# Performance work log

Hardware: AMD Instinct MI355X
Metric: run time of the kernel (lower is better)

The kernel has to match this reference:

```python
import jax, jax.numpy as jnp
import numpy as np

B, L, C, H = 32, 641, 768, 12
MEM = 128  # memory slots K; state token at index K; tokens are causal after that


def _block_mask(L, K):
    # rows i attend to cols j per FusedAttention:
    #  memory rows (i<K): attend to memory+state (j<=K)
    #  state row (i==K): attends to everything
    #  token rows (i>K): attend to memory+state (j<=K) and causally to tokens (K<j<=i)
    i = jnp.arange(L)[:, None]
    j = jnp.arange(L)[None, :]
    mem_rows = (i < K) & (j <= K)
    state_row = (i == K)
    tok_rows = (i > K) & ((j <= K) | ((j > K) & (j <= i)))
    return mem_rows | state_row | tok_rows  # (L, L) bool


def setup_inputs() -> dict:
    key = jax.random.key(0)
    k1, k2, k3 = jax.random.split(key, 3)
    x = jax.random.normal(k1, (B, L, C), dtype=jnp.float32)
    W_attn = jax.random.normal(k2, (C, 3 * C), dtype=jnp.float32) * 0.02
    W_proj = jax.random.normal(k3, (C, C), dtype=jnp.float32) * 0.02
    return {"x": x, "W_attn": W_attn, "W_proj": W_proj, "mem_size": MEM}


def reference(x, W_attn, W_proj, mem_size):
    Bb, Ll, Cc = x.shape
    hd = Cc // H
    qkv = x @ W_attn  # (B, L, 3C)
    q, k, v = jnp.split(qkv, 3, axis=-1)
    # (B, H, L, hd)
    q = q.reshape(Bb, Ll, H, hd).transpose(0, 2, 1, 3)
    k = k.reshape(Bb, Ll, H, hd).transpose(0, 2, 1, 3)
    v = v.reshape(Bb, Ll, H, hd).transpose(0, 2, 1, 3)
    mask = _block_mask(Ll, mem_size)  # (L, L)
    scale = 1.0 / jnp.sqrt(jnp.asarray(hd, dtype=x.dtype))
    att = jnp.einsum("bhqd,bhkd->bhqk", q, k) * scale
    att = jnp.where(mask[None, None, :, :], att, jnp.asarray(-jnp.inf, att.dtype))
    att = jax.nn.softmax(att, axis=-1)
    y = jnp.einsum("bhqk,bhkd->bhqd", att, v)
    y = y.transpose(0, 2, 1, 3).reshape(Bb, Ll, Cc)
    return y @ W_proj
```

## Files before the change

kernel.cpp:

```cpp
#include <hip/hip_runtime.h>
#include <stdint.h>

#define B_SZ 32
#define L_SZ 641
#define C_SZ 768
#define H_SZ 12
#define HD 64
#define MEMK 128
#define M_REAL (B_SZ * L_SZ)
#define M_PAD 20608
#define N_QKV (3 * C_SZ)
#define NQP 6
#define QK_STRIDE 1536
#define VT_STRIDE 648
#define SCL_LOG2E 0.18033688f
#define FIXED_MAX 8.0f

typedef __attribute__((ext_vector_type(8))) short short8;
typedef __attribute__((ext_vector_type(4))) float f32x4;
typedef __attribute__((ext_vector_type(4))) unsigned short ushort4v;

__device__ inline unsigned short f2bf(float x) {
  union { float f; uint32_t u; } v; v.f = x;
  uint32_t r = v.u + 0x7fffu + ((v.u >> 16) & 1u);
  return (unsigned short)(r >> 16);
}
__device__ inline float bf2f(short v) {
  union { float f; uint32_t u; } x; x.u = ((uint32_t)(unsigned short)v) << 16;
  return x.f;
}

__device__ inline void gload_lds16(const void* g, void* l) {
  __builtin_amdgcn_global_load_lds(
      (const __attribute__((address_space(1))) uint32_t*)g,
      (__attribute__((address_space(3))) uint32_t*)l, 16, 0, 0);
}

__global__ __launch_bounds__(256) void k_conv_x(const float* __restrict__ src,
                                                unsigned short* __restrict__ dst,
                                                int n4) {
  int i = blockIdx.x * 256 + threadIdx.x;
  if (i >= n4) return;
  float4 v = *(const float4*)(src + (size_t)i * 4);
  ushort4v o = { f2bf(v.x), f2bf(v.y), f2bf(v.z), f2bf(v.w) };
  int m = (unsigned)i / 192u;
  int k = (i - m * 192) * 4;
  int kk = k ^ ((m & 7) << 3);
  *(ushort4v*)(dst + (size_t)m * C_SZ + kk) = o;
}

__global__ __launch_bounds__(256) void k_transpose_bf16(const float* __restrict__ src,
                                                        unsigned short* __restrict__ dst,
                                                        int R, int Ccol,
                                                        float scale, int scale_cmax) {
  __shared__ float tile[32][33];
  int c0 = blockIdx.x * 32, r0 = blockIdx.y * 32;
  int tx = threadIdx.x & 31, ty = threadIdx.x >> 5;
  for (int i = ty; i < 32; i += 8)
    tile[i][tx] = src[(size_t)(r0 + i) * Ccol + c0 + tx];
  __syncthreads();
  float sc = (c0 < scale_cmax) ? scale : 1.0f;
  for (int i = ty; i < 32; i += 8) {
    int c = c0 + i;
    int r = (r0 + tx) ^ ((c & 7) << 3);
    dst[(size_t)c * R + r] = f2bf(tile[tx][i] * sc);
  }
}

template <int MODE>
__global__ __launch_bounds__(256) void k_gemm(const short* __restrict__ A,
                                              const short* __restrict__ Bt,
                                              void* __restrict__ Cp,
                                              short* __restrict__ vt,
                                              int Mreal, int N, int K) {
  __shared__ short As[2][128 * 64];
  __shared__ short Bs[2][128 * 64];
  int nwg = gridDim.x;
  int qq = nwg >> 3, rr = nwg & 7;
  int x8 = blockIdx.x & 7, i8 = blockIdx.x >> 3;
  int wg = (x8 < rr ? x8 * (qq + 1) : rr * (qq + 1) + (x8 - rr) * qq) + i8;
  const int tiles_n = N >> 7;
  int tm = wg / tiles_n, tn = wg % tiles_n;
  int m0 = tm << 7, n0 = tn << 7;
  int lane = threadIdx.x & 63, wave = threadIdx.x >> 6;
  int wr = wave >> 1, wc = wave & 1;
  int l15 = lane & 15, g = lane >> 4;
  int gswz = (l15 & 7) << 4;

  f32x4 acc[4][4];
  f32x4 z = {0.f, 0.f, 0.f, 0.f};
#pragma unroll
  for (int i = 0; i < 4; ++i)
#pragma unroll
    for (int j = 0; j < 4; ++j) acc[i][j] = z;

  int arow = lane >> 3;
  int acol = (lane & 7) * 8;

#define STAGE(K0, BUF)                                                        \
  {                                                                           \
    _Pragma("unroll")                                                         \
    for (int cc = 0; cc < 4; ++cc) {                                          \
      int rb = (cc * 4 + wave) * 8;                                           \
      gload_lds16(A + (size_t)(m0 + rb + arow) * K + ((K0) + acol),           \
                  (char*)As[BUF] + rb * 128);                                 \
      gload_lds16(Bt + (size_t)(n0 + rb + arow) * K + ((K0) + acol),          \
                  (char*)Bs[BUF] + rb * 128);                                 \
    }                                                                         \
  }

  STAGE(0, 0);
  STAGE(64, 1);
  int nk = K >> 6;
  for (int t = 0; t < nk; ++t) {
    int buf = t & 1;
    if (t + 1 < nk) {
      asm volatile("s_waitcnt vmcnt(8)" ::: "memory");
    } else {
      asm volatile("s_waitcnt vmcnt(0)" ::: "memory");
    }
    __builtin_amdgcn_s_barrier();
#pragma unroll
    for (int ks = 0; ks < 2; ++ks) {
      short8 a[4], b[4];
      int roff = (ks * 64) ^ gswz;
      if (MODE == 3) {
#pragma unroll
        for (int nf = 0; nf < 4; ++nf)
          a[nf] = *(const short8*)((char*)Bs[buf] +
                      (wr * 64 + nf * 16 + l15) * 128 + (roff ^ (g * 16)));
#pragma unroll
        for (int mf = 0; mf < 4; ++mf)
          b[mf] = *(const short8*)((char*)As[buf] +
                      (wc * 64 + mf * 16 + l15) * 128 + (roff ^ (g * 16)));
      } else {
#pragma unroll
        for (int mf = 0; mf < 4; ++mf)
          a[mf] = *(const short8*)((char*)As[buf] +
                      (wr * 64 + mf * 16 + l15) * 128 + (roff ^ (g * 16)));
#pragma unroll
        for (int nf = 0; nf < 4; ++nf)
          b[nf] = *(const short8*)((char*)Bs[buf] +
                      (wc * 64 + nf * 16 + l15) * 128 + (roff ^ (g * 16)));
      }
#pragma unroll
      for (int i = 0; i < 4; ++i)
#pragma unroll
        for (int j = 0; j < 4; ++j)
          acc[i][j] = __builtin_amdgcn_mfma_f32_16x16x32_bf16(a[i], b[j], acc[i][j], 0, 0, 0);
    }
    __builtin_amdgcn_s_barrier();
    __builtin_amdgcn_sched_barrier(0);
    if (t + 2 < nk) STAGE((t + 2) << 6, buf);
  }
#undef STAGE

  if (MODE == 3) {
#pragma unroll
    for (int nf = 0; nf < 4; ++nf) {
#pragma unroll
      for (int reg = 0; reg < 4; ++reg) {
        int n = n0 + wr * 64 + nf * 16 + g * 4 + reg;
        int h = n >> 6, d = n & 63;
        int xr = (d & 7) << 3;
#pragma unroll
        for (int mf = 0; mf < 4; ++mf) {
          int m = m0 + wc * 64 + mf * 16 + l15;
          if (m >= Mreal) continue;
          int bb = (unsigned)m / 641u;
          int key = m - bb * 641;
          int k2 = (key >= 640) ? key : (key ^ xr);
          vt[((size_t)(bb * H_SZ + h) * HD + d) * VT_STRIDE + k2] = f2bf(acc[nf][mf][reg]);
        }
      }
    }
    return;
  }
#pragma unroll
  for (int mf = 0; mf < 4; ++mf) {
#pragma unroll
    for (int reg = 0; reg < 4; ++reg) {
      int m = m0 + wr * 64 + mf * 16 + g * 4 + reg;
      if (m >= Mreal) continue;
      int xr = 0;
      if (MODE == 2) {
        int bb = (unsigned)m / 641u;
        int key = m - bb * 641;
        xr = (key & 7) << 3;
      }
#pragma unroll
      for (int nf = 0; nf < 4; ++nf) {
        int n = n0 + wc * 64 + nf * 16 + l15;
        float v = acc[mf][nf][reg];
        if (MODE == 2) {
          int nn = (n >= C_SZ) ? (n ^ xr) : n;
          ((unsigned short*)Cp)[(size_t)m * QK_STRIDE + nn] = f2bf(v);
        } else
          ((float*)Cp)[(size_t)m * N + n] = v;
      }
    }
  }
}

__global__ __launch_bounds__(512) void k_attn(const short* __restrict__ qk,
                                              const short* __restrict__ vt,
                                              short* __restrict__ y) {
  __shared__ short Ks[2][64 * 64];
  __shared__ short Vt[2][64 * 64];
  __shared__ short Ps[8][16 * 64];

  int bid = blockIdx.x;
  int work = (bid & 7) * 288 + (bid >> 3);
  int qp = work % NQP;
  int rem = work / NQP;
  int h = rem % H_SZ;
  int b = rem / H_SZ;
  int q0 = qp * 128;
  int tid = threadIdx.x;
  int lane = tid & 63, w = tid >> 6;
  int wgp = w >> 2;
  int l15 = lane & 15, g = lane >> 4;
  int q0w = q0 + wgp * 64 + (w & 3) * 16;

  size_t qbase = (size_t)(b * L_SZ + q0w + l15) * QK_STRIDE + h * HD;
  short8 qa[2];
#pragma unroll
  for (int ks = 0; ks < 2; ++ks)
    qa[ks] = *(const short8*)&qk[qbase + ks * 32 + g * 8];

  f32x4 o[4];
  float l_run[4];
  f32x4 z = {0.f, 0.f, 0.f, 0.f};
  f32x4 m8 = {-FIXED_MAX, -FIXED_MAX, -FIXED_MAX, -FIXED_MAX};
#pragma unroll
  for (int df = 0; df < 4; ++df) o[df] = z;
#pragma unroll
  for (int r = 0; r < 4; ++r) l_run[r] = 0.f;

  int jmax[4];
#pragma unroll
  for (int reg = 0; reg < 4; ++reg) {
    int i = q0w + g * 4 + reg;
    jmax[reg] = (i == MEMK) ? (L_SZ - 1) : (i < MEMK ? MEMK : i);
  }
  int jm_min = (q0w <= MEMK) ? MEMK : q0w;

  int q1 = q0 + 127; if (q1 > L_SZ - 1) q1 = L_SZ - 1;
  int col_max = (q0 <= MEMK && MEMK <= q1) ? (L_SZ - 1) : (q1 < MEMK ? MEMK : q1);
  int qw1 = q0w + 15;
  bool dead = (q0w >= L_SZ);
  int wcol = (q0w <= MEMK && MEMK <= qw1) ? (L_SZ - 1) : (qw1 < MEMK ? MEMK : qw1);
  if (dead) wcol = -1;

  size_t kbase = (size_t)b * L_SZ * QK_STRIDE + C_SZ + h * HD;
  size_t vbase = (size_t)(b * H_SZ + h) * HD * VT_STRIDE;

  int i0 = tid >> 3, j0e = (tid & 7) * 8;
  int rswz = (l15 & 7) << 4;

#define STAGE_ATTN(C0, BUF)                                                   \
  {                                                                           \
    gload_lds16(qk + kbase + (size_t)((C0) + i0) * QK_STRIDE + j0e,           \
                (char*)Ks[BUF] + w * 1024);                                   \
    gload_lds16(vt + vbase + (size_t)i0 * VT_STRIDE + (C0) + j0e,             \
                (char*)Vt[BUF] + w * 1024);                                   \
  }

  STAGE_ATTN(0, 0);
  STAGE_ATTN(64, 1);

  int nt = col_max >> 6;
  for (int t = 0; t <= nt; ++t) {
    int c0 = t << 6;
    int buf = t & 1;
    if (t + 1 <= nt) {
      asm volatile("s_waitcnt vmcnt(2)" ::: "memory");
    } else {
      asm volatile("s_waitcnt vmcnt(0)" ::: "memory");
    }
    __builtin_amdgcn_s_barrier();

    if (c0 <= wcol) {
      int vswz = (c0 >= 640) ? 0 : rswz;

      f32x4 s[4];
      __builtin_amdgcn_s_setprio(1);
#pragma unroll
      for (int kf = 0; kf < 4; ++kf) {
        f32x4 sa = m8;
#pragma unroll
        for (int ks = 0; ks < 2; ++ks) {
          short8 kb = *(const short8*)((char*)Ks[buf] +
                          (kf * 16 + l15) * 128 + ((ks * 64 + g * 16) ^ rswz));
          sa = __builtin_amdgcn_mfma_f32_16x16x32_bf16(qa[ks], kb, sa, 0, 0, 0);
        }
        s[kf] = sa;
      }
      __builtin_amdgcn_s_setprio(0);

      if (c0 + 63 > jm_min) {
#pragma unroll
        for (int kf = 0; kf < 4; ++kf) {
          int j = c0 + kf * 16 + l15;
#pragma unroll
          for (int reg = 0; reg < 4; ++reg)
            s[kf][reg] = (j <= jmax[reg]) ? s[kf][reg] : -1e30f;
        }
      }

#pragma unroll
      for (int kf = 0; kf < 4; ++kf)
#pragma unroll
        for (int reg = 0; reg < 4; ++reg)
          s[kf][reg] = exp2f(s[kf][reg]);
#pragma unroll
      for (int reg = 0; reg < 4; ++reg)
        l_run[reg] += (s[0][reg] + s[1][reg]) + (s[2][reg] + s[3][reg]);

#pragma unroll
      for (int reg = 0; reg < 4; ++reg) {
        int q = g * 4 + reg;
        char* prow = (char*)Ps[w] + q * 128;
        int qswz = (q & 7) << 4;
#pragma unroll
        for (int kf = 0; kf < 4; kf += 2) {
          uint32_t r;
          asm("v_cvt_pk_bf16_f32 %0, %1, %2"
              : "=v"(r) : "v"(s[kf][reg]), "v"(s[kf + 1][reg]));
          *(short*)(prow + ((kf * 32 + l15 * 2) ^ qswz)) = (short)(r & 0xffff);
          *(short*)(prow + (((kf + 1) * 32 + l15 * 2) ^ qswz)) = (short)(r >> 16);
        }
      }

      short8 pa[2];
#pragma unroll
      for (int ks = 0; ks < 2; ++ks)
        pa[ks] = *(const short8*)((char*)Ps[w] + l15 * 128 + ((ks * 64 + g * 16) ^ rswz));
      __builtin_amdgcn_s_setprio(1);
#pragma unroll
      for (int df = 0; df < 4; ++df) {
#pragma unroll
        for (int ks = 0; ks < 2; ++ks) {
          short8 vb = *(const short8*)((char*)Vt[buf] +
                          (df * 16 + l15) * 128 + ((ks * 64 + g * 16) ^ vswz));
          o[df] = __builtin_amdgcn_mfma_f32_16x16x32_bf16(pa[ks], vb, o[df], 0, 0, 0);
        }
      }
      __builtin_amdgcn_s_setprio(0);
    }

    __builtin_amdgcn_s_barrier();
    __builtin_amdgcn_sched_barrier(0);
    if (t + 2 <= nt) STAGE_ATTN((t + 2) << 6, buf);
  }
#undef STAGE_ATTN

#pragma unroll
  for (int reg = 0; reg < 4; ++reg) {
    float ls = l_run[reg];
    ls += __shfl_xor(ls, 1);
    ls += __shfl_xor(ls, 2);
    ls += __shfl_xor(ls, 4);
    ls += __shfl_xor(ls, 8);
    int i = q0w + g * 4 + reg;
    if (i >= L_SZ) continue;
    float inv = 1.0f / ls;
    size_t m = (size_t)(b * L_SZ + i);
    int ixr = ((int)(m & 7)) << 3;
#pragma unroll
    for (int df = 0; df < 4; ++df) {
      int col = (df * 16 + l15) ^ ixr;
      y[m * C_SZ + h * HD + col] = (short)f2bf(o[df][reg] * inv);
    }
  }
}

extern "C" void kernel_launch(void* const* d_in, const int* in_sizes, int n_in,
                              void* d_out, int out_size, void* d_ws, size_t ws_size,
                              hipStream_t stream) {
  const float* x = (const float*)d_in[0];
  const float* Wa = (const float*)d_in[1];
  const float* Wp = (const float*)d_in[2];
  float* out = (float*)d_out;

  char* ws = (char*)d_ws;
  size_t off0 = 0;
  short* x_bf = (short*)(ws + off0);
  size_t off1 = off0 + (size_t)M_PAD * C_SZ * 2;
  short* Wa_t = (short*)(ws + off1);
  size_t off2 = off1 + (size_t)N_QKV * C_SZ * 2;
  short* Wp_t = (short*)(ws + off2);
  size_t off3 = off2 + (size_t)C_SZ * C_SZ * 2;
  short* qk = (short*)(ws + off3);
  size_t off4 = off3 + (size_t)M_REAL * QK_STRIDE * 2;
  short* vt = (short*)(ws + off4);
  size_t need = off4 + (size_t)B_SZ * H_SZ * HD * VT_STRIDE * 2 + 4096;
  if (ws_size < need) return;

  int n4 = M_REAL * C_SZ / 4;
  k_conv_x<<<(n4 + 255) / 256, 256, 0, stream>>>(x, (unsigned short*)x_bf, n4);
  k_transpose_bf16<<<dim3(N_QKV / 32, C_SZ / 32), 256, 0, stream>>>(
      Wa, (unsigned short*)Wa_t, C_SZ, N_QKV, SCL_LOG2E, C_SZ);
  k_transpose_bf16<<<dim3(C_SZ / 32, C_SZ / 32), 256, 0, stream>>>(
      Wp, (unsigned short*)Wp_t, C_SZ, C_SZ, 1.0f, 0);

  k_gemm<2><<<(M_PAD / 128) * (QK_STRIDE / 128), 256, 0, stream>>>(
      x_bf, Wa_t, (void*)qk, nullptr, M_REAL, QK_STRIDE, C_SZ);
  k_gemm<3><<<(M_PAD / 128) * (C_SZ / 128), 256, 0, stream>>>(
      x_bf, Wa_t + (size_t)QK_STRIDE * C_SZ, nullptr, vt, M_REAL, C_SZ, C_SZ);
  k_attn<<<B_SZ * H_SZ * NQP, 512, 0, stream>>>(qk, vt, x_bf );
  k_gemm<0><<<(M_PAD / 128) * (C_SZ / 128), 256, 0, stream>>>(
      x_bf, Wp_t, (void*)out, nullptr, M_REAL, C_SZ, C_SZ);
}
```

Baseline: 242.2 us.

## Enlarge GEMM tiles to 256x256 with 512-thread workgroups

The shared GEMM kernel moves from 128x128 tiles with 4 waves to 256x256 tiles with 8 waves. Each wave now computes a 128x64 sub-tile, and A rows past M_PAD are clamped. The larger tiles raise arithmetic intensity and cut global and LDS traffic per FLOP. In exchange, LDS use rises to 128KB per block, each wave holds more accumulator registers, and the grid has far fewer workgroups, which risks lower occupancy and poor wave quantization across the CUs.

```diff
diff --git a/kernel.cpp b/kernel.cpp
--- a/kernel.cpp
+++ b/kernel.cpp
@@ -9,6 +9,7 @@
 #define MEMK 128
 #define M_REAL (B_SZ * L_SZ)
 #define M_PAD 20608
+#define MT256 81
 #define N_QKV (3 * C_SZ)
 #define NQP 6
 #define QK_STRIDE 1536
@@ -68,44 +69,46 @@
 }
 
 template <int MODE>
-__global__ __launch_bounds__(256) void k_gemm(const short* __restrict__ A,
-                                              const short* __restrict__ Bt,
-                                              void* __restrict__ Cp,
-                                              short* __restrict__ vt,
-                                              int Mreal, int N, int K) {
-  __shared__ short As[2][128 * 64];
-  __shared__ short Bs[2][128 * 64];
+__global__ __launch_bounds__(512, 2) void k_gemm(const short* __restrict__ A,
+                                                 const short* __restrict__ Bt,
+                                                 void* __restrict__ Cp,
+                                                 short* __restrict__ vt,
+                                                 int Mreal, int N, int K) {
+  __shared__ short As[2][256 * 64];
+  __shared__ short Bs[2][256 * 64];
   int nwg = gridDim.x;
   int qq = nwg >> 3, rr = nwg & 7;
   int x8 = blockIdx.x & 7, i8 = blockIdx.x >> 3;
   int wg = (x8 < rr ? x8 * (qq + 1) : rr * (qq + 1) + (x8 - rr) * qq) + i8;
-  const int tiles_n = N >> 7;
+  const int tiles_n = N >> 8;
   int tm = wg / tiles_n, tn = wg % tiles_n;
-  int m0 = tm << 7, n0 = tn << 7;
-  int lane = threadIdx.x & 63, wave = threadIdx.x >> 6;
-  int wr = wave >> 1, wc = wave & 1;
+  int m0 = tm << 8, n0 = tn << 8;
+  int tid = threadIdx.x;
+  int lane = tid & 63, wave = tid >> 6;
+  int wr = wave >> 2, wc = wave & 3;
   int l15 = lane & 15, g = lane >> 4;
   int gswz = (l15 & 7) << 4;
 
-  f32x4 acc[4][4];
+  f32x4 acc[8][4];
   f32x4 z = {0.f, 0.f, 0.f, 0.f};
 #pragma unroll
-  for (int i = 0; i < 4; ++i)
-#pragma unroll
-    for (int j = 0; j < 4; ++j) acc[i][j] = z;
-
-  int arow = lane >> 3;
-  int acol = (lane & 7) * 8;
+  for (int i2 = 0; i2 < 8; ++i2)
+#pragma unroll
+    for (int j2 = 0; j2 < 4; ++j2) acc[i2][j2] = z;
+
+  int srow = wave * 8 + (lane >> 3);
+  int scol = (lane & 7) * 8;
 
 #define STAGE(K0, BUF)                                                        \
   {                                                                           \
     _Pragma("unroll")                                                         \
-    for (int cc = 0; cc < 4; ++cc) {                                          \
-      int rb = (cc * 4 + wave) * 8;                                           \
-      gload_lds16(A + (size_t)(m0 + rb + arow) * K + ((K0) + acol),           \
-                  (char*)As[BUF] + rb * 128);                                 \
-      gload_lds16(Bt + (size_t)(n0 + rb + arow) * K + ((K0) + acol),          \
-                  (char*)Bs[BUF] + rb * 128);                                 \
+    for (int s = 0; s < 4; ++s) {                                             \
+      int ar = m0 + s * 64 + srow;                                            \
+      if (ar >= M_PAD) ar = M_PAD - 1;      \
+      gload_lds16(A + (size_t)ar * K + ((K0) + scol),                         \
+                  (char*)As[BUF] + s * 8192 + wave * 1024);                   \
+      gload_lds16(Bt + (size_t)(n0 + s * 64 + srow) * K + ((K0) + scol),      \
+                  (char*)Bs[BUF] + s * 8192 + wave * 1024);                   \
     }                                                                         \
   }
 
@@ -122,29 +125,28 @@
     __builtin_amdgcn_s_barrier();
 #pragma unroll
     for (int ks = 0; ks < 2; ++ks) {
-      short8 a[4], b[4];
-      int roff = (ks * 64) ^ gswz;
+      short8 a[8], b[4];
       if (MODE == 3) {
 #pragma unroll
-        for (int nf = 0; nf < 4; ++nf)
-          a[nf] = *(const short8*)((char*)Bs[buf] +
-                      (wr * 64 + nf * 16 + l15) * 128 + (roff ^ (g * 16)));
-#pragma unroll
-        for (int mf = 0; mf < 4; ++mf)
-          b[mf] = *(const short8*)((char*)As[buf] +
-                      (wc * 64 + mf * 16 + l15) * 128 + (roff ^ (g * 16)));
+        for (int j = 0; j < 8; ++j)
+          a[j] = *(const short8*)((char*)Bs[buf] +
+                      (wr * 128 + j * 16 + l15) * 128 + ((ks * 64 + g * 16) ^ gswz));
+#pragma unroll
+        for (int i = 0; i < 4; ++i)
+          b[i] = *(const short8*)((char*)As[buf] +
+                      (wc * 64 + i * 16 + l15) * 128 + ((ks * 64 + g * 16) ^ gswz));
       } else {
 #pragma unroll
-        for (int mf = 0; mf < 4; ++mf)
+        for (int mf = 0; mf < 8; ++mf)
           a[mf] = *(const short8*)((char*)As[buf] +
-                      (wr * 64 + mf * 16 + l15) * 128 + (roff ^ (g * 16)));
+                      (wr * 128 + mf * 16 + l15) * 128 + ((ks * 64 + g * 16) ^ gswz));
 #pragma unroll
         for (int nf = 0; nf < 4; ++nf)
           b[nf] = *(const short8*)((char*)Bs[buf] +
-                      (wc * 64 + nf * 16 + l15) * 128 + (roff ^ (g * 16)));
-      }
-#pragma unroll
-      for (int i = 0; i < 4; ++i)
+                      (wc * 64 + nf * 16 + l15) * 128 + ((ks * 64 + g * 16) ^ gswz));
+      }
+#pragma unroll
+      for (int i = 0; i < 8; ++i)
 #pragma unroll
         for (int j = 0; j < 4; ++j)
           acc[i][j] = __builtin_amdgcn_mfma_f32_16x16x32_bf16(a[i], b[j], acc[i][j], 0, 0, 0);
@@ -157,30 +159,30 @@
 
   if (MODE == 3) {
 #pragma unroll
-    for (int nf = 0; nf < 4; ++nf) {
+    for (int j = 0; j < 8; ++j) {
 #pragma unroll
       for (int reg = 0; reg < 4; ++reg) {
-        int n = n0 + wr * 64 + nf * 16 + g * 4 + reg;
+        int n = n0 + wr * 128 + j * 16 + g * 4 + reg;
         int h = n >> 6, d = n & 63;
         int xr = (d & 7) << 3;
 #pragma unroll
-        for (int mf = 0; mf < 4; ++mf) {
-          int m = m0 + wc * 64 + mf * 16 + l15;
+        for (int i = 0; i < 4; ++i) {
+          int m = m0 + wc * 64 + i * 16 + l15;
           if (m >= Mreal) continue;
           int bb = (unsigned)m / 641u;
           int key = m - bb * 641;
           int k2 = (key >= 640) ? key : (key ^ xr);
-          vt[((size_t)(bb * H_SZ + h) * HD + d) * VT_STRIDE + k2] = f2bf(acc[nf][mf][reg]);
+          vt[((size_t)(bb * H_SZ + h) * HD + d) * VT_STRIDE + k2] = f2bf(acc[j][i][reg]);
         }
       }
     }
     return;
   }
 #pragma unroll
-  for (int mf = 0; mf < 4; ++mf) {
+  for (int mf = 0; mf < 8; ++mf) {
 #pragma unroll
     for (int reg = 0; reg < 4; ++reg) {
-      int m = m0 + wr * 64 + mf * 16 + g * 4 + reg;
+      int m = m0 + wr * 128 + mf * 16 + g * 4 + reg;
       if (m >= Mreal) continue;
       int xr = 0;
       if (MODE == 2) {
@@ -404,11 +406,11 @@
   k_transpose_bf16<<<dim3(C_SZ / 32, C_SZ / 32), 256, 0, stream>>>(
       Wp, (unsigned short*)Wp_t, C_SZ, C_SZ, 1.0f, 0);
 
-  k_gemm<2><<<(M_PAD / 128) * (QK_STRIDE / 128), 256, 0, stream>>>(
+  k_gemm<2><<<MT256 * (QK_STRIDE / 256), 512, 0, stream>>>(
       x_bf, Wa_t, (void*)qk, nullptr, M_REAL, QK_STRIDE, C_SZ);
-  k_gemm<3><<<(M_PAD / 128) * (C_SZ / 128), 256, 0, stream>>>(
+  k_gemm<3><<<MT256 * (C_SZ / 256), 512, 0, stream>>>(
       x_bf, Wa_t + (size_t)QK_STRIDE * C_SZ, nullptr, vt, M_REAL, C_SZ, C_SZ);
   k_attn<<<B_SZ * H_SZ * NQP, 512, 0, stream>>>(qk, vt, x_bf );
-  k_gemm<0><<<(M_PAD / 128) * (C_SZ / 128), 256, 0, stream>>>(
+  k_gemm<0><<<MT256 * (C_SZ / 256), 512, 0, stream>>>(
       x_bf, Wp_t, (void*)out, nullptr, M_REAL, C_SZ, C_SZ);
 }
```

New measurement: 229.9 us. 1.05x faster.
